# Kernel tuning notes

Hardware: AMD Instinct MI355X
Metric: run time of the kernel (lower is better)

The kernel has to match this reference:

```python
import jax, jax.numpy as jnp
import numpy as np

B, PANO, OBJ, CFG, LM, IMG, D = 64, 36, 36, 16, 8, 32, 300
H, EMB, ANG, FEAT = 512, 64, 128, 2176
TOPN = 3
EPS = 1e-8


def setup_inputs() -> dict:
    key = jax.random.key(0)
    ks = jax.random.split(key, 24)
    f = lambda i, shape: jax.random.normal(ks[i], shape, dtype=jnp.float32)
    u = lambda i, shape: jax.random.uniform(ks[i], shape, dtype=jnp.float32)
    s = 0.02
    return {
        "action": f(0, (B, ANG)),
        "feature": f(1, (B, PANO, FEAT)),
        "cand_feat": f(2, (B, IMG, FEAT)),
        "prev_h1": f(3, (B, H)),
        "c_0": f(4, (B, H)),
        "ctx": f(5, (B, CFG, H)),
        "s_0": u(6, (B, CFG)),
        "landmark_object_feature": f(7, (B, CFG, LM, D)),
        "candidate_obj_text_feat": f(8, (B, IMG, OBJ, D)),
        "landmark_mask": u(9, (B, CFG, LM)),
        "landmark_relation": f(10, (B, CFG, LM, 6)),
        "landmark_relation_mask": u(11, (B, CFG, LM)),
        "candidate_relation": f(12, (B, IMG, 6)),
        "pano_obj_feat": f(13, (B, PANO, OBJ, D)),
        "emb_W": f(14, (ANG, EMB)) * s,
        "emb_b": jnp.zeros((EMB,), jnp.float32),
        "W_ih": f(15, (EMB + FEAT + TOPN * D, 4 * H)) * s,
        "W_hh": f(16, (H, 4 * H)) * s,
        "b_lstm": jnp.zeros((4 * H,), jnp.float32),
        "feat_in_W": f(17, (H, FEAT + TOPN * D)) * s,
        "att_in_W": f(18, (H, H)) * s,
        "att_out_W": f(19, (2 * H, H)) * s,
        "cand_in_W": f(20, (H, FEAT + TOPN * 7 + TOPN * D)) * s,
        "ctx_mask": jnp.zeros((B, CFG), dtype=bool),
    }


def _cos_argmax(obj_feat, land_flat):
    # obj_feat: [B,I,O,D], land_flat: [B,M,D] -> argmax over O of cosine sim: [B,I,M]
    dot = jnp.einsum('biod,bmd->biom', obj_feat, land_flat)
    na = jnp.linalg.norm(obj_feat, axis=-1)
    nb = jnp.linalg.norm(land_flat, axis=-1)
    sim = dot / jnp.maximum(na[..., None] * nb[:, None, None, :], EPS)
    return jnp.argmax(sim, axis=2)


def reference(action, feature, cand_feat, prev_h1, c_0, ctx, s_0,
              landmark_object_feature, candidate_obj_text_feat, landmark_mask,
              landmark_relation, landmark_relation_mask, candidate_relation,
              pano_obj_feat, emb_W, emb_b, W_ih, W_hh, b_lstm, feat_in_W,
              att_in_W, att_out_W, cand_in_W, ctx_mask):
    M = CFG * LM
    land_flat = landmark_object_feature.reshape(B, M, D)

    # --- pano object retrieval (cosine argmax + top-N config*landmark gather) ---
    pano_idx = _cos_argmax(pano_obj_feat, land_flat)                   # [B,36,M]
    top_idx = jax.lax.top_k((s_0[..., None] * landmark_mask).reshape(B, M), TOPN)[1]  # [B,3]
    sel = jnp.take_along_axis(pano_idx, jnp.broadcast_to(top_idx[:, None, :], (B, PANO, TOPN)), axis=2)
    pano_sim_obj = jnp.take_along_axis(
        pano_obj_feat, jnp.broadcast_to(sel[..., None], (B, PANO, TOPN, D)), axis=2
    ).reshape(B, PANO, TOPN * D)

    # --- embed action, feature attention (dropout = identity in eval) ---
    action_embeds = jnp.tanh(action @ emb_W + emb_b)
    feat_all = jnp.concatenate([feature, pano_sim_obj], axis=-1)       # [B,36,FEAT+900]
    a = jnp.einsum('bsd,bd->bs', feat_all, prev_h1 @ feat_in_W)
    p = jax.nn.softmax(a, axis=-1)
    attn_feat = jnp.einsum('bs,bsd->bd', p, feat_all)

    # --- LSTM cell ---
    gates = jnp.concatenate([action_embeds, attn_feat], axis=-1) @ W_ih + prev_h1 @ W_hh + b_lstm
    i_g, f_g, g_g, o_g = jnp.split(gates, 4, axis=-1)
    c_1 = jax.nn.sigmoid(f_g) * c_0 + jax.nn.sigmoid(i_g) * jnp.tanh(g_g)
    h_1 = jax.nn.sigmoid(o_g) * jnp.tanh(c_1)

    # --- ctx attention with mask + tilde ---
    lg = jnp.einsum('bsd,bd->bs', ctx, h_1 @ att_in_W)
    lg = jnp.where(ctx_mask, -jnp.inf, lg)
    ctx_attn = jax.nn.softmax(lg, axis=-1)
    wctx = jnp.einsum('bs,bsd->bd', ctx_attn, ctx)
    h_tilde = jnp.tanh(jnp.concatenate([wctx, h_1], axis=-1) @ att_out_W)

    # --- candidate object retrieval ---
    cand_idx = _cos_argmax(candidate_obj_text_feat, land_flat)         # [B,IMG,M]
    ctop = jax.lax.top_k((ctx_attn[..., None] * landmark_mask).reshape(B, M), TOPN)[1]
    land_rel_top = jnp.take_along_axis(landmark_relation.reshape(B, M, 6),
                                       jnp.broadcast_to(ctop[..., None], (B, TOPN, 6)), axis=1)
    land_obj_rel = jnp.einsum('bik,bjk->bij', candidate_relation, land_rel_top)   # [B,IMG,3]
    rel_mask_top = jnp.take_along_axis(landmark_relation_mask.reshape(B, M), ctop, axis=1)  # [B,3]
    csel = jnp.take_along_axis(cand_idx, jnp.broadcast_to(ctop[:, None, :], (B, IMG, TOPN)), axis=2)
    candi_sim_obj = jnp.take_along_axis(
        candidate_obj_text_feat, jnp.broadcast_to(csel[..., None], (B, IMG, TOPN, D)), axis=2)
    candi_rel = candidate_relation[:, :, None, :] * rel_mask_top[:, None, :, None]  # [B,IMG,3,6]
    new_feat = jnp.concatenate(
        [candi_sim_obj, jnp.concatenate([candi_rel, land_obj_rel[..., None]], axis=-1)],
        axis=-1).reshape(B, IMG, TOPN * (D + 7))
    cand_all = jnp.concatenate([cand_feat, new_feat], axis=-1)

    logit = jnp.einsum('bsd,bd->bs', cand_all, h_tilde @ cand_in_W)
    return h_1, c_1, logit, h_tilde, ctx_attn
```

## Files before the change

### kernel.cpp

```cpp
#include <hip/hip_runtime.h>
#include <math.h>

#define B_    64
#define PANO_ 36
#define OBJ_  36
#define CFG_  16
#define LM_   8
#define IMG_  32
#define D_    300
#define H_    512
#define EMB_  64
#define ANG_  128
#define FEAT_ 2176
#define M_    128

__device__ __forceinline__ float sigmoidf(float x) { return 1.0f / (1.0f + expf(-x)); }
__device__ __forceinline__ float dot4(float4 a, float4 b) {
    return a.x * b.x + a.y * b.y + a.z * b.z + a.w * b.w;
}
__device__ __forceinline__ float4 add4(float4 a, float4 b) {
    return make_float4(a.x + b.x, a.y + b.y, a.z + b.z, a.w + b.w);
}
__device__ __forceinline__ float4 fma4(float s, float4 a, float4 acc) {
    return make_float4(acc.x + s * a.x, acc.y + s * a.y, acc.z + s * a.z, acc.w + s * a.w);
}
__device__ __forceinline__ float4 ld4(const float* p) { return *reinterpret_cast<const float4*>(p); }

template <int TWO_SEG, int VEC_B>
__global__ __launch_bounds__(256)
void gemm_part(const float* __restrict__ A0, int lda0, int K0, const float* __restrict__ W0,
               const float* __restrict__ A1, int lda1, int K1, const float* __restrict__ W1,
               float* __restrict__ part, int N, int kchunk) {
    __shared__ __align__(16) float As[64][36];
    __shared__ __align__(16) float Bs[32][68];
    const int K = K0 + (TWO_SEG ? K1 : 0);
    int n0 = blockIdx.x * 64;
    int k0 = blockIdx.y * kchunk;
    if (k0 >= K) return;
    int kend = min(K, k0 + kchunk);
    int tid = threadIdx.x;
    int tr = tid >> 4, tc = tid & 15;
    float4 rA4[2];
    float4 rB4[2];
    float rB[8];
    float acc[4][4] = {};

    auto loadA = [&](int kb) {
#pragma unroll
        for (int l = 0; l < 2; l++) {
            int idx = tid + 256 * l;
            int r = idx >> 3, kq = idx & 7;
            int k = kb + 4 * kq;
            float4 v = make_float4(0.f, 0.f, 0.f, 0.f);
            if (k < kend) {
                const float* src = (TWO_SEG && k >= K0)
                    ? A1 + (size_t)r * lda1 + (k - K0)
                    : A0 + (size_t)r * lda0 + k;
                v = ld4(src);
            }
            rA4[l] = v;
        }
    };
    auto loadB = [&](int kb) {
        if (VEC_B) {
#pragma unroll
            for (int l = 0; l < 2; l++) {
                int idx = tid + 256 * l;
                int kk = idx >> 4, c4 = idx & 15;
                int k = kb + kk, n = n0 + 4 * c4;
                float4 v = make_float4(0.f, 0.f, 0.f, 0.f);
                if (k < kend && n < N) {
                    const float* src = (TWO_SEG && k >= K0)
                        ? W1 + (size_t)(k - K0) * N + n
                        : W0 + (size_t)k * N + n;
                    v = ld4(src);
                }
                rB4[l] = v;
            }
        } else {
#pragma unroll
            for (int l = 0; l < 8; l++) {
                int idx = tid + 256 * l;
                int kk = idx >> 6, c = idx & 63;
                int k = kb + kk, n = n0 + c;
                float v = 0.f;
                if (k < kend && n < N) {
                    v = (TWO_SEG && k >= K0) ? W1[(size_t)(k - K0) * N + n]
                                             : W0[(size_t)k * N + n];
                }
                rB[l] = v;
            }
        }
    };
    auto storeLDS = [&]() {
#pragma unroll
        for (int l = 0; l < 2; l++) {
            int idx = tid + 256 * l;
            *reinterpret_cast<float4*>(&As[idx >> 3][4 * (idx & 7)]) = rA4[l];
        }
        if (VEC_B) {
#pragma unroll
            for (int l = 0; l < 2; l++) {
                int idx = tid + 256 * l;
                *reinterpret_cast<float4*>(&Bs[idx >> 4][4 * (idx & 15)]) = rB4[l];
            }
        } else {
#pragma unroll
            for (int l = 0; l < 8; l++) {
                int idx = tid + 256 * l;
                Bs[idx >> 6][idx & 63] = rB[l];
            }
        }
    };
    auto compute = [&]() {
#pragma unroll
        for (int kk0 = 0; kk0 < 32; kk0 += 4) {
            float4 a0 = ld4(&As[4 * tr + 0][kk0]);
            float4 a1 = ld4(&As[4 * tr + 1][kk0]);
            float4 a2 = ld4(&As[4 * tr + 2][kk0]);
            float4 a3 = ld4(&As[4 * tr + 3][kk0]);
            float4 b0 = ld4(&Bs[kk0 + 0][4 * tc]);
            float4 b1 = ld4(&Bs[kk0 + 1][4 * tc]);
            float4 b2 = ld4(&Bs[kk0 + 2][4 * tc]);
            float4 b3 = ld4(&Bs[kk0 + 3][4 * tc]);
#define ROWFMA(i, ai) \
            acc[i][0] += ai.x * b0.x + ai.y * b1.x + ai.z * b2.x + ai.w * b3.x; \
            acc[i][1] += ai.x * b0.y + ai.y * b1.y + ai.z * b2.y + ai.w * b3.y; \
            acc[i][2] += ai.x * b0.z + ai.y * b1.z + ai.z * b2.z + ai.w * b3.z; \
            acc[i][3] += ai.x * b0.w + ai.y * b1.w + ai.z * b2.w + ai.w * b3.w;
            ROWFMA(0, a0) ROWFMA(1, a1) ROWFMA(2, a2) ROWFMA(3, a3)
#undef ROWFMA
        }
    };

    loadA(k0); loadB(k0);
    storeLDS();
    __syncthreads();
    for (int kb = k0 + 32; kb < kend; kb += 32) {
        loadA(kb); loadB(kb);
        compute();
        __syncthreads();
        storeLDS();
        __syncthreads();
    }
    compute();

    float* outp = part + (size_t)blockIdx.y * 64 * N;
    if (VEC_B) {
#pragma unroll
        for (int i = 0; i < 4; i++) {
            int r = 4 * tr + i;
            int n = n0 + 4 * tc;
            if (n < N)
                *reinterpret_cast<float4*>(outp + (size_t)r * N + n) =
                    make_float4(acc[i][0], acc[i][1], acc[i][2], acc[i][3]);
        }
    } else {
#pragma unroll
        for (int i = 0; i < 4; i++) {
            int r = 4 * tr + i;
#pragma unroll
            for (int j = 0; j < 4; j++) {
                int n = n0 + 4 * tc + j;
                if (n < N) outp[(size_t)r * N + n] = acc[i][j];
            }
        }
    }
}

__global__ void reduce4_kernel(const float4* __restrict__ part, int S, int total4,
                               float4* __restrict__ out) {
    int i = blockIdx.x * 256 + threadIdx.x;
    if (i >= total4) return;
    float4 v = make_float4(0.f, 0.f, 0.f, 0.f);
    for (int s = 0; s < S; s++) v = add4(v, part[(size_t)s * total4 + i]);
    out[i] = v;
}

__global__ void reduce_remap_kernel(const float* __restrict__ part, int S,
                                    float* __restrict__ out) {
    int b = blockIdx.y;
    int c = blockIdx.x * 256 + threadIdx.x;
    if (c >= 3097) return;
    float v = 0.f;
    for (int s = 0; s < S; s++) v += part[(size_t)s * (B_ * 3097) + (size_t)b * 3097 + c];
    int oc;
    if (c < 2176) oc = c;
    else { int u = c - 2176; oc = 2176 + (u / 307) * 308 + (u % 307); }
    out[(size_t)b * 3104 + oc] = v;
}

__global__ void tanh_reduce_kernel(const float4* __restrict__ part, int S,
                                   float4* __restrict__ htld, float4* __restrict__ out_ht) {
    int i = blockIdx.x * 256 + threadIdx.x;
    if (i >= B_ * H_ / 4) return;
    float4 v = make_float4(0.f, 0.f, 0.f, 0.f);
    for (int s = 0; s < S; s++) v = add4(v, part[(size_t)s * (B_ * H_ / 4) + i]);
    float4 t = make_float4(tanhf(v.x), tanhf(v.y), tanhf(v.z), tanhf(v.w));
    htld[i] = t;
    out_ht[i] = t;
}

__global__ __launch_bounds__(256)
void pano_logits_kernel(const float* __restrict__ pobj,
                        const float* __restrict__ land,
                        const float* __restrict__ s0,
                        const float* __restrict__ lmask,
                        const float* __restrict__ feature,
                        const float* __restrict__ qfeat,
                        int* __restrict__ sel,
                        float* __restrict__ aval) {
    __shared__ __align__(16) float land3[3][304];
    __shared__ int mids[3];
    __shared__ float simv[3][40];
    __shared__ float redV[2];
    __shared__ int redI[2];
    __shared__ int fin[3];
    __shared__ float wred[4];
    int i = blockIdx.x, b = blockIdx.y, tid = threadIdx.x;
    int wave = tid >> 6, lane = tid & 63;

    float tv; int tm;
    if (tid < 128) { tv = s0[b * CFG_ + (tid >> 3)] * lmask[(size_t)b * M_ + tid]; tm = tid; }
    else { tv = -INFINITY; tm = 1 << 30; }
    for (int t = 0; t < 3; t++) {
        float bv = tv; int bi = tm;
        for (int off = 32; off >= 1; off >>= 1) {
            float ov = __shfl_xor(bv, off);
            int   oi = __shfl_xor(bi, off);
            if (ov > bv || (ov == bv && oi < bi)) { bv = ov; bi = oi; }
        }
        if (lane == 0 && wave < 2) { redV[wave] = bv; redI[wave] = bi; }
        __syncthreads();
        if (tid == 0)
            mids[t] = (redV[0] > redV[1] || (redV[0] == redV[1] && redI[0] < redI[1])) ? redI[0] : redI[1];
        __syncthreads();
        if (tm == mids[t]) tv = -INFINITY;
    }

    for (int idx = tid; idx < 912; idx += 256) {
        int t = idx / 304, k = idx % 304;
        land3[t][k] = (k < 300) ? land[((size_t)b * 128 + mids[t]) * 300 + k] : 0.f;
    }
    __syncthreads();

    const float* obase = pobj + (((size_t)b * 36 + i) * 36) * 300;
    const float* qf = qfeat + (size_t)b * 3076;
    const float* frow = feature + ((size_t)b * 36 + i) * 2176;
    float facc = 0.f;

    if (tid < 144) {
        int g = tid >> 2, gl = tid & 3;
        const float* row = obase + (size_t)g * 300;
        float c0 = 0, c1 = 0, c2 = 0, sn = 0;
        float4 a = ld4(row + 4 * gl);
        for (int k4 = gl; k4 < 75; k4 += 4) {
            float4 cur = a;
            int kn = k4 + 4;
            if (kn < 75) a = ld4(row + 4 * kn);
            float4 l0 = ld4(&land3[0][4 * k4]);
            float4 l1 = ld4(&land3[1][4 * k4]);
            float4 l2 = ld4(&land3[2][4 * k4]);
            sn += dot4(cur, cur);
            c0 += dot4(cur, l0);
            c1 += dot4(cur, l1);
            c2 += dot4(cur, l2);
        }
#pragma unroll
        for (int off = 1; off <= 2; off <<= 1) {
            c0 += __shfl_xor(c0, off);
            c1 += __shfl_xor(c1, off);
            c2 += __shfl_xor(c2, off);
            sn += __shfl_xor(sn, off);
        }
        if (gl == 0) {
            float inv = 1.0f / sqrtf(fmaxf(sn, 1e-20f));
            simv[0][g] = c0 * inv;
            simv[1][g] = c1 * inv;
            simv[2][g] = c2 * inv;
        }
    } else {
        for (int d4 = tid - 144; d4 < 544; d4 += 112)
            facc += dot4(ld4(frow + 4 * d4), ld4(qf + 4 * d4));
    }
    __syncthreads();
    if (tid < 3) {
        float bv = -INFINITY; int bo = 0;
        for (int o2 = 0; o2 < 36; o2++) {
            float v = simv[tid][o2];
            if (v > bv) { bv = v; bo = o2; }
        }
        fin[tid] = bo;
        sel[((size_t)b * 36 + i) * 3 + tid] = bo;
    }
    __syncthreads();

    float acc = facc;
    for (int idx = tid; idx < 225; idx += 256) {
        int t = idx / 75, k4 = idx % 75;
        acc += dot4(ld4(obase + (size_t)fin[t] * 300 + 4 * k4),
                    ld4(qf + 2176 + t * 300 + 4 * k4));
    }
    for (int off = 32; off >= 1; off >>= 1) acc += __shfl_xor(acc, off);
    if (lane == 0) wred[wave] = acc;
    __syncthreads();
    if (tid == 0) aval[b * 36 + i] = wred[0] + wred[1] + wred[2] + wred[3];
}

__global__ __launch_bounds__(256)
void attn_wsum_kernel(const float* __restrict__ feature,
                      const float* __restrict__ pobj,
                      const int* __restrict__ sel,
                      const float* __restrict__ aval,
                      const float* __restrict__ action,
                      const float* __restrict__ embW,
                      const float* __restrict__ embB,
                      float* __restrict__ xcat) {
    __shared__ float lg[36];
    __shared__ float pe[36];
    __shared__ int ss[36][3];
    int b = blockIdx.y, tid = threadIdx.x;
    int d4 = blockIdx.x * 256 + tid;
    if (tid < 36) lg[tid] = aval[b * 36 + tid];
    for (int idx = tid; idx < 108; idx += 256) ss[idx / 3][idx % 3] = sel[(size_t)b * 108 + idx];
    __syncthreads();
    float mx = -INFINITY;
    for (int s = 0; s < 36; s++) mx = fmaxf(mx, lg[s]);
    if (tid < 36) pe[tid] = expf(lg[tid] - mx);
    __syncthreads();
    float sum = 0;
    for (int s = 0; s < 36; s++) sum += pe[s];
    float invS = 1.0f / sum;
    if (d4 < 769) {
        float4 acc = make_float4(0.f, 0.f, 0.f, 0.f);
        if (d4 < 544) {
            const float* fb = feature + (size_t)b * 36 * 2176 + 4 * d4;
            for (int s = 0; s < 36; s++) acc = fma4(pe[s], ld4(fb + (size_t)s * 2176), acc);
        } else {
            int u = d4 - 544, t = u / 75, k4 = u % 75;
            const float* pb = pobj + (size_t)b * 36 * 36 * 300;
            for (int s = 0; s < 36; s++)
                acc = fma4(pe[s], ld4(pb + ((size_t)s * 36 + ss[s][t]) * 300 + 4 * k4), acc);
        }
        acc = make_float4(acc.x * invS, acc.y * invS, acc.z * invS, acc.w * invS);
        *reinterpret_cast<float4*>(xcat + (size_t)b * 3140 + 64 + 4 * d4) = acc;
    }
    if (blockIdx.x == 0 && tid < 64) {
        float acc = embB[tid];
        for (int k = 0; k < ANG_; k++)
            acc += action[b * ANG_ + k] * embW[k * EMB_ + tid];
        xcat[(size_t)b * 3140 + tid] = tanhf(acc);
    }
}

__global__ void lstm_kernel(const float* __restrict__ gp, int S,
                            const float* __restrict__ b_lstm,
                            const float* __restrict__ c0,
                            float* __restrict__ out_h1,
                            float* __restrict__ out_c1) {
    int idx4 = blockIdx.x * 256 + threadIdx.x;
    if (idx4 >= B_ * H_ / 4) return;
    int b = idx4 >> 7;
    int d4 = idx4 & 127;
    float4 ig = ld4(b_lstm + 4 * d4);
    float4 fg = ld4(b_lstm + 512 + 4 * d4);
    float4 gg = ld4(b_lstm + 1024 + 4 * d4);
    float4 og = ld4(b_lstm + 1536 + 4 * d4);
    for (int s = 0; s < S; s++) {
        const float* g = gp + (size_t)s * (B_ * 2048) + (size_t)b * 2048 + 4 * d4;
        ig = add4(ig, ld4(g));
        fg = add4(fg, ld4(g + 512));
        gg = add4(gg, ld4(g + 1024));
        og = add4(og, ld4(g + 1536));
    }
    float4 cv = ld4(c0 + 4 * idx4);
    float4 c1, h1;
    c1.x = sigmoidf(fg.x) * cv.x + sigmoidf(ig.x) * tanhf(gg.x);
    c1.y = sigmoidf(fg.y) * cv.y + sigmoidf(ig.y) * tanhf(gg.y);
    c1.z = sigmoidf(fg.z) * cv.z + sigmoidf(ig.z) * tanhf(gg.z);
    c1.w = sigmoidf(fg.w) * cv.w + sigmoidf(ig.w) * tanhf(gg.w);
    h1.x = sigmoidf(og.x) * tanhf(c1.x);
    h1.y = sigmoidf(og.y) * tanhf(c1.y);
    h1.z = sigmoidf(og.z) * tanhf(c1.z);
    h1.w = sigmoidf(og.w) * tanhf(c1.w);
    *reinterpret_cast<float4*>(out_c1 + 4 * idx4) = c1;
    *reinterpret_cast<float4*>(out_h1 + 4 * idx4) = h1;
}

__global__ __launch_bounds__(256)
void ctx_attn_kernel(const float* __restrict__ ctx,
                     const float* __restrict__ qctx_part,
                     const float* __restrict__ h1f,
                     const float* __restrict__ lmask,
                     float* __restrict__ ccbuf,
                     float* __restrict__ out_attn,
                     int* __restrict__ ctop) {
    __shared__ __align__(16) float qc[512];
    __shared__ float part[16][17];
    __shared__ float lgv[16];
    __shared__ float att[16];
    __shared__ float redV[2];
    __shared__ int redI[2];
    __shared__ int mids[3];
    int b = blockIdx.x, tid = threadIdx.x;
    int wave = tid >> 6, lane = tid & 63;
    if (tid < 128) {
        float4 v = make_float4(0.f, 0.f, 0.f, 0.f);
#pragma unroll
        for (int s = 0; s < 8; s++)
            v = add4(v, ld4(qctx_part + (size_t)s * (B_ * 512) + (size_t)b * 512 + 4 * tid));
        *reinterpret_cast<float4*>(&qc[4 * tid]) = v;
    }
    __syncthreads();
    int s = tid >> 4, l = tid & 15;
    float acc = 0;
    for (int d = l; d < 512; d += 16) acc += ctx[((size_t)b * 16 + s) * 512 + d] * qc[d];
    part[s][l] = acc;
    __syncthreads();
    if (tid < 16) {
        float sum = 0;
        for (int j = 0; j < 16; j++) sum += part[tid][j];
        lgv[tid] = sum;
    }
    __syncthreads();
    if (tid < 16) {
        float mx = -INFINITY;
        for (int j = 0; j < 16; j++) mx = fmaxf(mx, lgv[j]);
        att[tid] = expf(lgv[tid] - mx);
    }
    __syncthreads();
    float sum = 0;
    for (int j = 0; j < 16; j++) sum += att[j];
    float invS = 1.0f / sum;
    if (tid < 16) out_attn[b * 16 + tid] = att[tid] * invS;
    for (int d = tid; d < 512; d += 256) {
        float acc2 = 0;
        for (int sj = 0; sj < 16; sj++)
            acc2 += att[sj] * ctx[((size_t)b * 16 + sj) * 512 + d];
        ccbuf[(size_t)b * 1024 + d] = acc2 * invS;
        ccbuf[(size_t)b * 1024 + 512 + d] = h1f[(size_t)b * 512 + d];
    }
    float tv; int tm;
    if (tid < 128) { tv = att[tid >> 3] * lmask[(size_t)b * M_ + tid]; tm = tid; }
    else { tv = -INFINITY; tm = 1 << 30; }
    for (int t = 0; t < 3; t++) {
        float bv = tv; int bi = tm;
        for (int off = 32; off >= 1; off >>= 1) {
            float ov = __shfl_xor(bv, off);
            int   oi = __shfl_xor(bi, off);
            if (ov > bv || (ov == bv && oi < bi)) { bv = ov; bi = oi; }
        }
        if (lane == 0 && wave < 2) { redV[wave] = bv; redI[wave] = bi; }
        __syncthreads();
        if (tid == 0) {
            int pick = (redV[0] > redV[1] || (redV[0] == redV[1] && redI[0] < redI[1])) ? redI[0] : redI[1];
            mids[t] = pick;
            ctop[b * 3 + t] = pick;
        }
        __syncthreads();
        if (tm == mids[t]) tv = -INFINITY;
    }
}

__global__ __launch_bounds__(256)
void cand_fused_kernel(const float* __restrict__ cobj,
                       const float* __restrict__ land,
                       const int* __restrict__ ctop,
                       const float* __restrict__ landrel,
                       const float* __restrict__ lrmask,
                       const float* __restrict__ crel_g,
                       const float* __restrict__ cand_feat,
                       const float* __restrict__ qcand,
                       float* __restrict__ out_logit) {
    __shared__ __align__(16) float land3[3][304];
    __shared__ float relL[3][6];
    __shared__ float relM[3];
    __shared__ float crel[6];
    __shared__ int mids[3];
    __shared__ float simv[3][40];
    __shared__ int fin[3];
    __shared__ float wsum[4];
    int img = blockIdx.x, b = blockIdx.y, tid = threadIdx.x;
    int wave = tid >> 6, lane = tid & 63;
    if (tid < 3) mids[tid] = ctop[b * 3 + tid];
    __syncthreads();
    for (int idx = tid; idx < 912; idx += 256) {
        int t = idx / 304, k = idx % 304;
        land3[t][k] = (k < 300) ? land[((size_t)b * 128 + mids[t]) * 300 + k] : 0.f;
    }
    if (tid < 18) { int t = tid / 6, k = tid % 6; relL[t][k] = landrel[((size_t)b * 128 + mids[t]) * 6 + k]; }
    if (tid >= 32 && tid < 35) { int t = tid - 32; relM[t] = lrmask[(size_t)b * 128 + mids[t]]; }
    if (tid >= 64 && tid < 70) { crel[tid - 64] = crel_g[((size_t)b * 32 + img) * 6 + (tid - 64)]; }
    __syncthreads();

    const float* obase = cobj + (((size_t)b * 32 + img) * 36) * 300;
    const float* q = qcand + (size_t)b * 3104;
    const float* cf = cand_feat + ((size_t)b * 32 + img) * 2176;
    float facc = 0.f;

    if (tid < 144) {
        int g = tid >> 2, gl = tid & 3;
        const float* row = obase + (size_t)g * 300;
        float c0 = 0, c1 = 0, c2 = 0, sn = 0;
        float4 a = ld4(row + 4 * gl);
        for (int k4 = gl; k4 < 75; k4 += 4) {
            float4 cur = a;
            int kn = k4 + 4;
            if (kn < 75) a = ld4(row + 4 * kn);
            float4 l0 = ld4(&land3[0][4 * k4]);
            float4 l1 = ld4(&land3[1][4 * k4]);
            float4 l2 = ld4(&land3[2][4 * k4]);
            sn += dot4(cur, cur);
            c0 += dot4(cur, l0);
            c1 += dot4(cur, l1);
            c2 += dot4(cur, l2);
        }
#pragma unroll
        for (int off = 1; off <= 2; off <<= 1) {
            c0 += __shfl_xor(c0, off);
            c1 += __shfl_xor(c1, off);
            c2 += __shfl_xor(c2, off);
            sn += __shfl_xor(sn, off);
        }
        if (gl == 0) {
            float inv = 1.0f / sqrtf(fmaxf(sn, 1e-20f));
            simv[0][g] = c0 * inv;
            simv[1][g] = c1 * inv;
            simv[2][g] = c2 * inv;
        }
    } else {
        for (int d4 = tid - 144; d4 < 544; d4 += 112)
            facc += dot4(ld4(cf + 4 * d4), ld4(q + 4 * d4));
    }
    __syncthreads();
    if (tid < 3) {
        float bv = -INFINITY; int bo = 0;
        for (int o2 = 0; o2 < 36; o2++) {
            float v = simv[tid][o2];
            if (v > bv) { bv = v; bo = o2; }
        }
        fin[tid] = bo;
    }
    __syncthreads();

    float acc = facc;
    for (int idx = tid; idx < 225; idx += 256) {
        int t = idx / 75, k4 = idx % 75;
        acc += dot4(ld4(obase + (size_t)fin[t] * 300 + 4 * k4),
                    ld4(q + 2176 + t * 308 + 4 * k4));
    }
    if (tid < 21) {
        int t = tid / 7, j = tid % 7;
        float val;
        if (j < 6) val = crel[j] * relM[t];
        else { val = 0; for (int k = 0; k < 6; k++) val += crel[k] * relL[t][k]; }
        acc += val * q[2176 + t * 308 + 300 + j];
    }
    for (int off = 32; off >= 1; off >>= 1) acc += __shfl_xor(acc, off);
    if (lane == 0) wsum[wave] = acc;
    __syncthreads();
    if (tid == 0) {
        out_logit[(size_t)b * 32 + img] = wsum[0] + wsum[1] + wsum[2] + wsum[3];
    }
}

extern "C" void kernel_launch(void* const* d_in, const int* in_sizes, int n_in,
                              void* d_out, int out_size, void* d_ws, size_t ws_size,
                              hipStream_t stream) {
    const float* action    = (const float*)d_in[0];
    const float* feature   = (const float*)d_in[1];
    const float* cand_feat = (const float*)d_in[2];
    const float* prev_h1   = (const float*)d_in[3];
    const float* c_0       = (const float*)d_in[4];
    const float* ctx       = (const float*)d_in[5];
    const float* s_0       = (const float*)d_in[6];
    const float* lobj      = (const float*)d_in[7];
    const float* cobj      = (const float*)d_in[8];
    const float* lmask     = (const float*)d_in[9];
    const float* lrel      = (const float*)d_in[10];
    const float* lrelmask  = (const float*)d_in[11];
    const float* crel      = (const float*)d_in[12];
    const float* pobj      = (const float*)d_in[13];
    const float* embW      = (const float*)d_in[14];
    const float* embB      = (const float*)d_in[15];
    const float* W_ih      = (const float*)d_in[16];
    const float* W_hh      = (const float*)d_in[17];
    const float* b_lstm    = (const float*)d_in[18];
    const float* feat_in_W = (const float*)d_in[19];
    const float* att_in_W  = (const float*)d_in[20];
    const float* att_out_W = (const float*)d_in[21];
    const float* cand_in_W = (const float*)d_in[22];

    float* ws = (float*)d_ws;
    float* gates_part = ws;
    float* qf_part    = gates_part + 2621440;
    float* q_feat     = qf_part + 1574912;
    float* qctx_part  = q_feat + 196864;
    float* htpre_part = qctx_part + 262144;
    float* htld       = htpre_part + 524288;
    float* qcand_part = htld + 32768;
    float* q_cand     = qcand_part + 1585664;
    float* xcat       = q_cand + 198656;
    float* ccbuf      = xcat + 200960;
    float* aval       = ccbuf + 65536;
    int*   ctop       = (int*)(aval + 2304);
    int*   sel        = ctop + 192;

    float* out       = (float*)d_out;
    float* out_h1    = out;
    float* out_c1    = out + 32768;
    float* out_logit = out + 65536;
    float* out_ht    = out + 67584;
    float* out_attn  = out + 100352;

    gemm_part<0, 1><<<dim3(49, 8), 256, 0, stream>>>(prev_h1, H_, H_, feat_in_W,
                                                     nullptr, 0, 0, nullptr,
                                                     qf_part, 3076, 64);
    reduce4_kernel<<<193, 256, 0, stream>>>((const float4*)qf_part, 8, 49216, (float4*)q_feat);

    pano_logits_kernel<<<dim3(PANO_, B_), 256, 0, stream>>>(pobj, lobj, s_0, lmask, feature, q_feat, sel, aval);

    attn_wsum_kernel<<<dim3(4, B_), 256, 0, stream>>>(feature, pobj, sel, aval, action, embW, embB, xcat);

    gemm_part<1, 1><<<dim3(32, 20), 256, 0, stream>>>(xcat, 3140, 3140, W_ih,
                                                      prev_h1, H_, H_, W_hh,
                                                      gates_part, 2048, 192);
    lstm_kernel<<<32, 256, 0, stream>>>(gates_part, 20, b_lstm, c_0, out_h1, out_c1);

    gemm_part<0, 1><<<dim3(8, 8), 256, 0, stream>>>(out_h1, H_, H_, att_in_W,
                                                    nullptr, 0, 0, nullptr,
                                                    qctx_part, H_, 64);
    ctx_attn_kernel<<<B_, 256, 0, stream>>>(ctx, qctx_part, out_h1, lmask, ccbuf, out_attn, ctop);

    gemm_part<0, 1><<<dim3(8, 16), 256, 0, stream>>>(ccbuf, 1024, 1024, att_out_W,
                                                     nullptr, 0, 0, nullptr,
                                                     htpre_part, H_, 64);
    tanh_reduce_kernel<<<32, 256, 0, stream>>>((const float4*)htpre_part, 16,
                                               (float4*)htld, (float4*)out_ht);

    gemm_part<0, 0><<<dim3(49, 8), 256, 0, stream>>>(htld, H_, H_, cand_in_W,
                                                     nullptr, 0, 0, nullptr,
                                                     qcand_part, 3097, 64);
    reduce_remap_kernel<<<dim3(13, B_), 256, 0, stream>>>(qcand_part, 8, q_cand);

    cand_fused_kernel<<<dim3(IMG_, B_), 256, 0, stream>>>(cobj, lobj, ctop, lrel, lrelmask,
                                                          crel, cand_feat, q_cand, out_logit);
}
```

Before: 449.0 us.

## Hoist per-batch top-3 selection out of pano blocks and rebalance cosine phase

Moves the per-batch top-3 landmark selection, previously recomputed redundantly by all 36 pano blocks per batch, into extra blocks of the existing reduction kernel. The pano blocks then just read the three indices. The cosine-similarity phase is factored into a shared helper that uses whole waves (192 threads), a 4-deep register prefetch buffer and fully unrolled loops. The feature dot now runs on exactly one wave with unrolled strided loads. The weighted-sum loops also get unroll pragmas. This cuts redundant work and barrier chains at the cost of more registers and a workspace buffer.

Measured after the change: 488.8 us. +8.9%, slower.

```diff
diff --git a/kernel.cpp b/kernel.cpp
--- a/kernel.cpp
+++ b/kernel.cpp
@@ -168,13 +168,45 @@
     }
 }
 
-__global__ void reduce4_kernel(const float4* __restrict__ part, int S, int total4,
-                               float4* __restrict__ out) {
-    int i = blockIdx.x * 256 + threadIdx.x;
-    if (i >= total4) return;
-    float4 v = make_float4(0.f, 0.f, 0.f, 0.f);
-    for (int s = 0; s < S; s++) v = add4(v, part[(size_t)s * total4 + i]);
-    out[i] = v;
+__global__ void reduce4_top3_kernel(const float4* __restrict__ part, int S, int total4,
+                                    float4* __restrict__ out,
+                                    const float* __restrict__ s0,
+                                    const float* __restrict__ lmask,
+                                    int* __restrict__ pmids) {
+    int tid = threadIdx.x;
+    if (blockIdx.x < 193) {
+        int i = blockIdx.x * 256 + tid;
+        if (i >= total4) return;
+        float4 v = make_float4(0.f, 0.f, 0.f, 0.f);
+        for (int s = 0; s < S; s++) v = add4(v, part[(size_t)s * total4 + i]);
+        out[i] = v;
+        return;
+    }
+    __shared__ float redV[2];
+    __shared__ int redI[2];
+    __shared__ int mids[3];
+    int b = blockIdx.x - 193;
+    int wave = tid >> 6, lane = tid & 63;
+    float tv; int tm;
+    if (tid < 128) { tv = s0[b * CFG_ + (tid >> 3)] * lmask[(size_t)b * M_ + tid]; tm = tid; }
+    else { tv = -INFINITY; tm = 1 << 30; }
+    for (int t = 0; t < 3; t++) {
+        float bv = tv; int bi = tm;
+        for (int off = 32; off >= 1; off >>= 1) {
+            float ov = __shfl_xor(bv, off);
+            int   oi = __shfl_xor(bi, off);
+            if (ov > bv || (ov == bv && oi < bi)) { bv = ov; bi = oi; }
+        }
+        if (lane == 0 && wave < 2) { redV[wave] = bv; redI[wave] = bi; }
+        __syncthreads();
+        if (tid == 0) {
+            int pick = (redV[0] > redV[1] || (redV[0] == redV[1] && redI[0] < redI[1])) ? redI[0] : redI[1];
+            mids[t] = pick;
+            pmids[b * 3 + t] = pick;
+        }
+        __syncthreads();
+        if (tm == mids[t]) tv = -INFINITY;
+    }
 }
 
 __global__ void reduce_remap_kernel(const float* __restrict__ part, int S,
@@ -201,11 +233,57 @@
     out_ht[i] = t;
 }
 
+template <typename F>
+__device__ __forceinline__ void cos_phase(int tid, const float* __restrict__ obase,
+                                          const float land3[3][304], float simv[3][40],
+                                          F&& dotBranch) {
+    if (tid < 192) {
+        int g = tid >> 2, gl = tid & 3;
+        if (g < 36) {
+            const float* row = obase + (size_t)g * 300;
+            float c0 = 0, c1 = 0, c2 = 0, sn = 0;
+            float4 buf[4];
+#pragma unroll
+            for (int p = 0; p < 4; p++) buf[p] = ld4(row + 4 * (gl + 4 * p));
+#pragma unroll
+            for (int j = 0; j < 19; j++) {
+                int k4 = gl + 4 * j;
+                if (k4 < 75) {
+                    float4 cur = buf[j & 3];
+                    int kn = gl + 4 * (j + 4);
+                    if (kn < 75) buf[j & 3] = ld4(row + 4 * kn);
+                    float4 l0 = ld4(&land3[0][4 * k4]);
+                    float4 l1 = ld4(&land3[1][4 * k4]);
+                    float4 l2 = ld4(&land3[2][4 * k4]);
+                    sn += dot4(cur, cur);
+                    c0 += dot4(cur, l0);
+                    c1 += dot4(cur, l1);
+                    c2 += dot4(cur, l2);
+                }
+            }
+#pragma unroll
+            for (int off = 1; off <= 2; off <<= 1) {
+                c0 += __shfl_xor(c0, off);
+                c1 += __shfl_xor(c1, off);
+                c2 += __shfl_xor(c2, off);
+                sn += __shfl_xor(sn, off);
+            }
+            if (gl == 0) {
+                float inv = 1.0f / sqrtf(fmaxf(sn, 1e-20f));
+                simv[0][g] = c0 * inv;
+                simv[1][g] = c1 * inv;
+                simv[2][g] = c2 * inv;
+            }
+        }
+    } else {
+        dotBranch(tid - 192);
+    }
+}
+
 __global__ __launch_bounds__(256)
 void pano_logits_kernel(const float* __restrict__ pobj,
                         const float* __restrict__ land,
-                        const float* __restrict__ s0,
-                        const float* __restrict__ lmask,
+                        const int* __restrict__ pmids,
                         const float* __restrict__ feature,
                         const float* __restrict__ qfeat,
                         int* __restrict__ sel,
@@ -213,31 +291,13 @@
     __shared__ __align__(16) float land3[3][304];
     __shared__ int mids[3];
     __shared__ float simv[3][40];
-    __shared__ float redV[2];
-    __shared__ int redI[2];
     __shared__ int fin[3];
     __shared__ float wred[4];
     int i = blockIdx.x, b = blockIdx.y, tid = threadIdx.x;
     int wave = tid >> 6, lane = tid & 63;
 
-    float tv; int tm;
-    if (tid < 128) { tv = s0[b * CFG_ + (tid >> 3)] * lmask[(size_t)b * M_ + tid]; tm = tid; }
-    else { tv = -INFINITY; tm = 1 << 30; }
-    for (int t = 0; t < 3; t++) {
-        float bv = tv; int bi = tm;
-        for (int off = 32; off >= 1; off >>= 1) {
-            float ov = __shfl_xor(bv, off);
-            int   oi = __shfl_xor(bi, off);
-            if (ov > bv || (ov == bv && oi < bi)) { bv = ov; bi = oi; }
-        }
-        if (lane == 0 && wave < 2) { redV[wave] = bv; redI[wave] = bi; }
-        __syncthreads();
-        if (tid == 0)
-            mids[t] = (redV[0] > redV[1] || (redV[0] == redV[1] && redI[0] < redI[1])) ? redI[0] : redI[1];
-        __syncthreads();
-        if (tm == mids[t]) tv = -INFINITY;
-    }
-
+    if (tid < 3) mids[tid] = pmids[b * 3 + tid];
+    __syncthreads();
     for (int idx = tid; idx < 912; idx += 256) {
         int t = idx / 304, k = idx % 304;
         land3[t][k] = (k < 300) ? land[((size_t)b * 128 + mids[t]) * 300 + k] : 0.f;
@@ -249,40 +309,14 @@
     const float* frow = feature + ((size_t)b * 36 + i) * 2176;
     float facc = 0.f;
 
-    if (tid < 144) {
-        int g = tid >> 2, gl = tid & 3;
-        const float* row = obase + (size_t)g * 300;
-        float c0 = 0, c1 = 0, c2 = 0, sn = 0;
-        float4 a = ld4(row + 4 * gl);
-        for (int k4 = gl; k4 < 75; k4 += 4) {
-            float4 cur = a;
-            int kn = k4 + 4;
-            if (kn < 75) a = ld4(row + 4 * kn);
-            float4 l0 = ld4(&land3[0][4 * k4]);
-            float4 l1 = ld4(&land3[1][4 * k4]);
-            float4 l2 = ld4(&land3[2][4 * k4]);
-            sn += dot4(cur, cur);
-            c0 += dot4(cur, l0);
-            c1 += dot4(cur, l1);
-            c2 += dot4(cur, l2);
-        }
-#pragma unroll
-        for (int off = 1; off <= 2; off <<= 1) {
-            c0 += __shfl_xor(c0, off);
-            c1 += __shfl_xor(c1, off);
-            c2 += __shfl_xor(c2, off);
-            sn += __shfl_xor(sn, off);
-        }
-        if (gl == 0) {
-            float inv = 1.0f / sqrtf(fmaxf(sn, 1e-20f));
-            simv[0][g] = c0 * inv;
-            simv[1][g] = c1 * inv;
-            simv[2][g] = c2 * inv;
-        }
-    } else {
-        for (int d4 = tid - 144; d4 < 544; d4 += 112)
-            facc += dot4(ld4(frow + 4 * d4), ld4(qf + 4 * d4));
-    }
+    cos_phase(tid, obase, land3, simv, [&](int l) {
+#pragma unroll
+        for (int j = 0; j < 9; j++) {
+            int d4 = l + 64 * j;
+            if (d4 < 544)
+                facc += dot4(ld4(frow + 4 * d4), ld4(qf + 4 * d4));
+        }
+    });
     __syncthreads();
     if (tid < 3) {
         float bv = -INFINITY; int bo = 0;
@@ -335,10 +369,12 @@
         float4 acc = make_float4(0.f, 0.f, 0.f, 0.f);
         if (d4 < 544) {
             const float* fb = feature + (size_t)b * 36 * 2176 + 4 * d4;
+#pragma unroll 4
             for (int s = 0; s < 36; s++) acc = fma4(pe[s], ld4(fb + (size_t)s * 2176), acc);
         } else {
             int u = d4 - 544, t = u / 75, k4 = u % 75;
             const float* pb = pobj + (size_t)b * 36 * 36 * 300;
+#pragma unroll 4
             for (int s = 0; s < 36; s++)
                 acc = fma4(pe[s], ld4(pb + ((size_t)s * 36 + ss[s][t]) * 300 + 4 * k4), acc);
         }
@@ -498,40 +534,14 @@
     const float* cf = cand_feat + ((size_t)b * 32 + img) * 2176;
     float facc = 0.f;
 
-    if (tid < 144) {
-        int g = tid >> 2, gl = tid & 3;
-        const float* row = obase + (size_t)g * 300;
-        float c0 = 0, c1 = 0, c2 = 0, sn = 0;
-        float4 a = ld4(row + 4 * gl);
-        for (int k4 = gl; k4 < 75; k4 += 4) {
-            float4 cur = a;
-            int kn = k4 + 4;
-            if (kn < 75) a = ld4(row + 4 * kn);
-            float4 l0 = ld4(&land3[0][4 * k4]);
-            float4 l1 = ld4(&land3[1][4 * k4]);
-            float4 l2 = ld4(&land3[2][4 * k4]);
-            sn += dot4(cur, cur);
-            c0 += dot4(cur, l0);
-            c1 += dot4(cur, l1);
-            c2 += dot4(cur, l2);
-        }
-#pragma unroll
-        for (int off = 1; off <= 2; off <<= 1) {
-            c0 += __shfl_xor(c0, off);
-            c1 += __shfl_xor(c1, off);
-            c2 += __shfl_xor(c2, off);
-            sn += __shfl_xor(sn, off);
-        }
-        if (gl == 0) {
-            float inv = 1.0f / sqrtf(fmaxf(sn, 1e-20f));
-            simv[0][g] = c0 * inv;
-            simv[1][g] = c1 * inv;
-            simv[2][g] = c2 * inv;
-        }
-    } else {
-        for (int d4 = tid - 144; d4 < 544; d4 += 112)
-            facc += dot4(ld4(cf + 4 * d4), ld4(q + 4 * d4));
-    }
+    cos_phase(tid, obase, land3, simv, [&](int l) {
+#pragma unroll
+        for (int j = 0; j < 9; j++) {
+            int d4 = l + 64 * j;
+            if (d4 < 544)
+                facc += dot4(ld4(cf + 4 * d4), ld4(q + 4 * d4));
+        }
+    });
     __syncthreads();
     if (tid < 3) {
         float bv = -INFINITY; int bo = 0;
@@ -605,6 +615,7 @@
     float* aval       = ccbuf + 65536;
     int*   ctop       = (int*)(aval + 2304);
     int*   sel        = ctop + 192;
+    int*   pmids      = sel + 6912;
 
     float* out       = (float*)d_out;
     float* out_h1    = out;
@@ -616,9 +627,10 @@
     gemm_part<0, 1><<<dim3(49, 8), 256, 0, stream>>>(prev_h1, H_, H_, feat_in_W,
                                                      nullptr, 0, 0, nullptr,
                                                      qf_part, 3076, 64);
-    reduce4_kernel<<<193, 256, 0, stream>>>((const float4*)qf_part, 8, 49216, (float4*)q_feat);
-
-    pano_logits_kernel<<<dim3(PANO_, B_), 256, 0, stream>>>(pobj, lobj, s_0, lmask, feature, q_feat, sel, aval);
+    reduce4_top3_kernel<<<257, 256, 0, stream>>>((const float4*)qf_part, 8, 49216,
+                                                 (float4*)q_feat, s_0, lmask, pmids);
+
+    pano_logits_kernel<<<dim3(PANO_, B_), 256, 0, stream>>>(pobj, lobj, pmids, feature, q_feat, sel, aval);
 
     attn_wsum_kernel<<<dim3(4, B_), 256, 0, stream>>>(feature, pobj, sel, aval, action, embW, embB, xcat);
 
```
